# Optimization experiments

Measured on AMD Instinct MI355X. Metric: run time of the kernel, lower is better.

The kernel has to match this reference:

```python
import jax, jax.numpy as jnp
import numpy as np

N = 262144   # cohort size (k_n)
M = 8192     # number of ordinal anchor indices (len(Hj))


def setup_inputs() -> dict:
    key = jax.random.key(0)
    k1, k2, k3, k4, k5 = jax.random.split(key, 5)
    time = jax.random.uniform(k1, (N,), dtype=jnp.float32) * 1000.0
    event = (jax.random.uniform(k2, (N,), dtype=jnp.float32) < 0.3).astype(jnp.float32)
    y_true0 = jnp.stack([time, event], axis=1)          # [N,2] (time, event)
    y_true1 = y_true0                                    # second head labels (unused by loss)
    y_pred0 = jax.random.normal(k3, (N, 1), dtype=jnp.float32) * 0.1  # xbeta head 0
    y_pred1 = jax.random.normal(k4, (N, 1), dtype=jnp.float32) * 0.1  # xbeta head 1
    Hj = jnp.sort(jax.random.randint(k5, (M,), 0, N, dtype=jnp.int32))  # static event indices into sorted order
    log_vars = jnp.zeros((2, 1), dtype=jnp.float32)      # layer weights log_var0, log_var1
    return {"y_true0": y_true0, "y_true1": y_true1, "y_pred0": y_pred0,
            "y_pred1": y_pred1, "Hj": Hj, "log_vars": log_vars}


def reference(y_true0, y_true1, y_pred0, y_pred1, Hj, log_vars):
    n = y_true0.shape[0]
    # top_k with k = n == full descending sort by time
    _, order = jax.lax.top_k(y_true0[:, 0], n)

    # ---- neg_log_pl (Cox negative partial log-likelihood, per-sample vector) ----
    xbeta = y_pred0[order, 0]                 # [N] sorted by descending time
    event = y_true0[order, 1]                 # [N]
    denom = jnp.cumsum(jnp.exp(xbeta))        # risk-set cumulative sum
    lossA = -(event * (xbeta - jnp.log(denom)))  # [N]

    # ---- ordinal_loss0 (pairwise ranking over event indices Hj in sorted order) ----
    # intended math: for each j, for ii >= j: cost += 1 - exp(xbeta[Hj[j]] - xbeta[Hj[ii]])
    xb = y_pred1[order, 0]                    # [N] sorted
    xh = xb[Hj]                               # [M]
    m = Hj.shape[0]
    rec = 1.0 - jnp.exp(xh[:, None] - xh[None, :])   # [M,M] rec[j,ii]
    mask = jnp.triu(jnp.ones((m, m), dtype=bool))    # ii >= j
    cost2 = jnp.sum(jnp.where(mask, rec, 0.0))

    # ---- multi_loss combination with learned log variances ----
    lv0 = log_vars[0, 0]
    lv1 = log_vars[1, 0]
    precision1 = jnp.clip(jnp.exp(-lv1), 0.0, 1.0)
    loss = jnp.sum(lossA + lv0) + (precision1 * cost2 + lv1)
    return loss


if __name__ == "__main__":
    out = reference(**setup_inputs())
    print(out)
```

## Files before the change

kernel.cpp:

```cpp
#include <hip/hip_runtime.h>
#include <math.h>


#define BSHIFT 12
#define NBUCK (1 << 19)
#define BLK 256
#define NC1 32
#define M40 ((1ull << 40) - 1)

#define BAR_FLAG 512
#define BAR_REL  1024

#define STORE_U32(p, v) __hip_atomic_store((p), (v), __ATOMIC_RELAXED, __HIP_MEMORY_SCOPE_AGENT)
#define STORE_F32(p, v) __hip_atomic_store((p), (v), __ATOMIC_RELAXED, __HIP_MEMORY_SCOPE_AGENT)
#define STORE_U64(p, v) __hip_atomic_store((unsigned long long*)(p), (v), __ATOMIC_RELAXED, __HIP_MEMORY_SCOPE_AGENT)
#define LOAD_U32(p) __hip_atomic_load((p), __ATOMIC_RELAXED, __HIP_MEMORY_SCOPE_AGENT)
#define FADD_U32(p, v) __hip_atomic_fetch_add((p), (v), __ATOMIC_RELAXED, __HIP_MEMORY_SCOPE_AGENT)

template <int GRID>
__device__ __forceinline__ void gbar(unsigned* bar, unsigned gv) {
  __syncthreads();
  constexpr unsigned BPC = GRID / NC1;
  const int t = threadIdx.x;
  const unsigned grp = blockIdx.x & (NC1 - 1);
  if (blockIdx.x == 0) {
    if (t == 0) {
      unsigned a = FADD_U32(bar + grp * 16, 1u);
      if (a == gv * BPC - 1u) STORE_U32(bar + BAR_FLAG + grp * 16, gv);
    }
    if (t < NC1) {
      int guard = 0;
      while (LOAD_U32(bar + BAR_FLAG + t * 16) < gv) {
        __builtin_amdgcn_s_sleep(1);
        if (++guard > 5000000) break;
      }
      STORE_U32(bar + BAR_REL + t * 16, gv);
    }
    __syncthreads();
  } else {
    if (t == 0) {
      unsigned a = FADD_U32(bar + grp * 16, 1u);
      if (a == gv * BPC - 1u) STORE_U32(bar + BAR_FLAG + grp * 16, gv);
      int guard = 0;
      while (LOAD_U32(bar + BAR_REL + grp * 16) < gv) {
        __builtin_amdgcn_s_sleep(1);
        if (++guard > 5000000) break;
      }
    }
    __syncthreads();
  }
}

template <int GRID>
__device__ __forceinline__ void gbar_last(unsigned* bar, unsigned gv) {
  __syncthreads();
  constexpr unsigned BPC = GRID / NC1;
  const int t = threadIdx.x;
  const unsigned grp = blockIdx.x & (NC1 - 1);
  if (blockIdx.x == 0) {
    if (t == 0) {
      unsigned a = FADD_U32(bar + grp * 16, 1u);
      if (a == gv * BPC - 1u) STORE_U32(bar + BAR_FLAG + grp * 16, gv);
    }
    if (t < NC1) {
      int guard = 0;
      while (LOAD_U32(bar + BAR_FLAG + t * 16) < gv) {
        __builtin_amdgcn_s_sleep(1);
        if (++guard > 5000000) break;
      }
    }
    __syncthreads();
  } else {
    if (t == 0) {
      unsigned a = FADD_U32(bar + grp * 16, 1u);
      if (a == gv * BPC - 1u) STORE_U32(bar + BAR_FLAG + grp * 16, gv);
    }
  }
}

__global__ void __launch_bounds__(BLK, 4)
k_hist(const float2* __restrict__ yt0, const float* __restrict__ yp0, int n,
       unsigned long long* __restrict__ rec, unsigned* __restrict__ seq) {
  int i = blockIdx.x * BLK + threadIdx.x;
  if (i >= n) return;
  float2 te = yt0[i];
  unsigned key = __float_as_uint(te.x);
  float e = expf(yp0[i]);
  unsigned long long qe = (unsigned long long)(e * 16777216.0f + 0.5f);
  if (qe > (1ull << 32)) qe = (1ull << 32);
  unsigned long long ret = atomicAdd(&rec[key >> BSHIFT], (1ull << 40) | qe);
  seq[i] = (unsigned)(ret >> 40);
}

template <int GRID>
__global__ void __launch_bounds__(BLK, 4)
k_scan(const unsigned long long* __restrict__ rec,
       const int* __restrict__ Hj, int m,
       unsigned* __restrict__ bar, unsigned* __restrict__ bitmap,
       unsigned long long* __restrict__ Epack,
       unsigned* __restrict__ bTot, float* __restrict__ fTot) {
  constexpr int TOT = GRID * BLK;
  constexpr int BPB = NBUCK / GRID;
  constexpr int BPT = BPB / BLK;
  const int t = threadIdx.x;
  const int g = blockIdx.x;
  const int gtid = g * BLK + t;

  __shared__ unsigned su[BLK];
  __shared__ float    sff[BLK];

  for (int j = gtid; j < m; j += TOT) {
    int h = Hj[j];
    atomicOr(&bitmap[h >> 5], 1u << (h & 31));
  }

  unsigned cK[BPT]; float fK[BPT];
  unsigned thrC; float thrF;
  {
    unsigned runc = 0u; float runf = 0.f;
    #pragma unroll
    for (int k = 0; k < BPT; ++k) {
      int b = NBUCK - 1 - (g * BPB + t * BPT + k);
      unsigned long long v = rec[b];
      cK[k] = (unsigned)(v >> 40);
      fK[k] = (float)((double)(v & M40) * (1.0 / 16777216.0));
      runc += cK[k]; runf += fK[k];
    }
    su[t] = runc; sff[t] = runf;
    __syncthreads();
    for (int off2 = 1; off2 < BLK; off2 <<= 1) {
      unsigned uc = (t >= off2) ? su[t - off2] : 0u;
      float    uf = (t >= off2) ? sff[t - off2] : 0.f;
      __syncthreads();
      su[t] += uc; sff[t] += uf;
      __syncthreads();
    }
    thrC = (t > 0) ? su[t - 1] : 0u;
    thrF = (t > 0) ? sff[t - 1] : 0.f;
    if (t == BLK - 1) { STORE_U32(&bTot[g], su[t]); STORE_F32(&fTot[g], sff[t]); }
  }
  gbar<GRID>(bar, 1);

  {
    unsigned partC = 0u; float partF = 0.f;
    for (int j = t; j < g; j += BLK) { partC += bTot[j]; partF += fTot[j]; }
    su[t] = partC; sff[t] = partF;
    __syncthreads();
    for (int s = BLK / 2; s > 0; s >>= 1) {
      if (t < s) { su[t] += su[t + s]; sff[t] += sff[t + s]; }
      __syncthreads();
    }
    unsigned baseC = su[0]; float baseF = sff[0];
    __syncthreads();
    unsigned preC = 0u; float preF = 0.f;
    #pragma unroll
    for (int k = 0; k < BPT; ++k) {
      int b = NBUCK - 1 - (g * BPB + t * BPT + k);
      unsigned sfxC = baseC + thrC + preC;
      float    sfxF = baseF + thrF + preF;
      Epack[b] = ((unsigned long long)__float_as_uint(sfxF) << 32) | sfxC;
      preC += cK[k]; preF += fK[k];
    }
  }
}

template <int GRID>
__global__ void __launch_bounds__(BLK, 4)
k_main(const float2* __restrict__ yt0, const float* __restrict__ yp0,
       const float* __restrict__ yp1, const int* __restrict__ Hj,
       const float* __restrict__ lv, int n, int m,
       unsigned* __restrict__ bar, const unsigned* __restrict__ seq,
       const unsigned* __restrict__ bitmap,
       const unsigned long long* __restrict__ Epack,
       uint2* __restrict__ skey2, unsigned* __restrict__ sidx,
       float* __restrict__ xh, double* __restrict__ accum,
       float* __restrict__ out) {
  constexpr int TOT = GRID * BLK;
  const int t = threadIdx.x;
  const int g = blockIdx.x;
  const int gtid = g * BLK + t;

  __shared__ double sd[BLK];
  __shared__ float  wt[4];

  #pragma unroll
  for (int el = 0; el < 2; ++el) {
    int i = gtid + el * TOT;
    if (i < n) {
      float2 te = yt0[i];
      unsigned key = __float_as_uint(te.x);
      unsigned ev = (te.y != 0.f) ? 0x80000000u : 0u;
      float e = expf(yp0[i]);
      unsigned b = key >> BSHIFT;
      unsigned start = ((const unsigned*)Epack)[2u * b];
      unsigned pos = start + seq[i];
      unsigned long long v =
          ((unsigned long long)__float_as_uint(e) << 32) | key;
      STORE_U64(&skey2[pos], v);
      STORE_U32(&sidx[pos], (unsigned)i | ev);
    }
  }
  gbar<GRID>(bar, 1);

  {
    double contrib = 0.0;
    #pragma unroll
    for (int el = 0; el < 2; ++el) {
      int p = gtid + el * TOT;
      if (p >= n) continue;
      uint2 kv = skey2[p];
      unsigned key = kv.x;
      float e = __uint_as_float(kv.y);
      unsigned sidv = sidx[p];
      unsigned idx = sidv & 0x7FFFFFFFu;
      bool evb = (sidv >> 31) != 0u;
      unsigned b = key >> BSHIFT;
      unsigned long long ep = Epack[b];
      unsigned start = (unsigned)ep;
      float cross = __uint_as_float((unsigned)(ep >> 32));
      unsigned end = (b > 0) ? ((const unsigned*)Epack)[2u * (b - 1)]
                             : (unsigned)n;
      if (end > (unsigned)n) end = (unsigned)n;
      if (start > end) start = end;
      float wsum = 0.f;
      unsigned wcnt = 0u;
      unsigned q = start;
      while (q + 8 <= end) {
        uint2 v[8];
        #pragma unroll
        for (int k = 0; k < 8; ++k) v[k] = skey2[q + k];
        #pragma unroll
        for (int k = 0; k < 8; ++k) {
          if (v[k].x > key) { wsum += __uint_as_float(v[k].y); wcnt++; }
          else if (v[k].x == key && (sidx[q + k] & 0x7FFFFFFFu) < idx) {
            wsum += __uint_as_float(v[k].y); wcnt++;
          }
        }
        q += 8;
      }
      for (; q < end; ++q) {
        uint2 v = skey2[q];
        if (v.x > key) { wsum += __uint_as_float(v.y); wcnt++; }
        else if (v.x == key && (sidx[q] & 0x7FFFFFFFu) < idx) {
          wsum += __uint_as_float(v.y); wcnt++;
        }
      }
      float denom = cross + wsum + e;
      int rank = (int)(start + wcnt);
      if (evb) contrib += (double)logf(denom / e);
      if ((bitmap[rank >> 5] >> (rank & 31)) & 1u) {
        int lo = 0, hi = m;
        while (lo < hi) { int mid = (lo + hi) >> 1; if (Hj[mid] < rank) lo = mid + 1; else hi = mid; }
        if (lo < m && Hj[lo] == rank) {
          float xb1 = yp1[idx];
          for (int j = lo; j < m && Hj[j] == rank; ++j) STORE_F32(&xh[j], xb1);
        }
      }
    }
    sd[t] = contrib;
    __syncthreads();
    for (int s = 128; s > 0; s >>= 1) { if (t < s) sd[t] += sd[t + s]; __syncthreads(); }
    if (t == 0) atomicAdd(accum, sd[0]);
  }
  gbar_last<GRID>(bar, 2);

  if (g != 0) return;
  {
    int lane = t & 63;
    int w = t >> 6;
    double acc = 0.0;
    float carry = 0.f;
    int passes = (m + 2047) / 2048;
    for (int pss = passes - 1; pss >= 0; --pss) {
      int base = pss * 2048 + t * 8;
      float x[8], eb[8];
      float c = 0.f;
      #pragma unroll
      for (int k = 0; k < 8; ++k) {
        int j = base + k;
        x[k] = (j < m) ? xh[j] : 0.f;
        eb[k] = (j < m) ? expf(-x[k]) : 0.f;
        c += eb[k];
      }
      float s = c;
      #pragma unroll
      for (int d = 1; d < 64; d <<= 1) {
        float o = __shfl_down(s, d, 64);
        if (lane + d < 64) s += o;
      }
      float wtot = __shfl(s, 0, 64);
      if (lane == 0) wt[w] = wtot;
      __syncthreads();
      float after = 0.f, ptot = 0.f;
      #pragma unroll
      for (int w2 = 0; w2 < 4; ++w2) { ptot += wt[w2]; if (w2 > w) after += wt[w2]; }
      float S = (s - c) + after + carry;
      #pragma unroll
      for (int k = 7; k >= 0; --k) {
        int j = base + k;
        S += eb[k];
        if (j < m) acc += (double)(expf(x[k]) * S);
      }
      __syncthreads();
      carry += ptot;
    }
    sd[t] = acc;
    __syncthreads();
    for (int s2 = 128; s2 > 0; s2 >>= 1) { if (t < s2) sd[t] += sd[t + s2]; __syncthreads(); }
    if (t == 0) {
      double T = (double)m * (double)(m + 1) * 0.5;
      double cost2 = T - sd[0];
      float lv0 = lv[0], lv1 = lv[1];
      float prec1 = fminf(expf(-lv1), 1.0f);
      double loss = *accum + (double)n * (double)lv0 + (double)prec1 * cost2 + (double)lv1;
      out[0] = (float)loss;
    }
  }
}

extern "C" void kernel_launch(void* const* d_in, const int* in_sizes, int n_in,
                              void* d_out, int out_size, void* d_ws, size_t ws_size,
                              hipStream_t stream) {
  (void)n_in; (void)out_size;
  const float2* yt0 = (const float2*)d_in[0];
  const float*  yp0 = (const float*)d_in[2];
  const float*  yp1 = (const float*)d_in[3];
  const int*    Hj  = (const int*)d_in[4];
  const float*  lv  = (const float*)d_in[5];
  int n = in_sizes[0] / 2;
  int m = in_sizes[4];

  char* ws = (char*)d_ws;
  unsigned* barS  = (unsigned*)ws;
  unsigned* barM  = (unsigned*)(ws + 8192);
  double*   accum = (double*)(ws + 16128);
  size_t off = 16384;
  auto alloc = [&](size_t bytes) -> void* {
    void* p = ws + off;
    off += (bytes + 255) & ~(size_t)255;
    return p;
  };
  size_t nbm = ((size_t)(n + 31) / 32) * 4;
  unsigned* bitmap = (unsigned*)alloc(nbm);
  unsigned long long* rec = (unsigned long long*)alloc((size_t)NBUCK * 8);
  size_t zbytes = off;
  unsigned long long* Epack = (unsigned long long*)alloc((size_t)NBUCK * 8);
  unsigned* bTot  = (unsigned*)alloc(1024 * 4);
  float*    fTot  = (float*)alloc(1024 * 4);
  unsigned* seq   = (unsigned*)alloc((size_t)n * 4);
  uint2*    skey2 = (uint2*)alloc((size_t)n * 8);
  unsigned* sidx  = (unsigned*)alloc((size_t)n * 4);
  float*    xh    = (float*)alloc((size_t)m * 4);
  if (off > ws_size) return;

  hipMemsetAsync(ws, 0, zbytes, stream);

  static int gridChoice = 0;
  if (gridChoice == 0) {
    int nb = 0;
    hipError_t e1 = hipOccupancyMaxActiveBlocksPerMultiprocessor(&nb, k_main<1024>, BLK, 0);
    int dev = 0; hipGetDevice(&dev);
    hipDeviceProp_t prop;
    hipError_t e2 = hipGetDeviceProperties(&prop, dev);
    gridChoice = (e1 == hipSuccess && e2 == hipSuccess &&
                  nb * prop.multiProcessorCount >= 1024) ? 1024 : 512;
  }

  int gHist = (n + BLK - 1) / BLK;
  k_hist<<<dim3(gHist), dim3(BLK), 0, stream>>>(yt0, yp0, n, rec, seq);
  if (gridChoice == 1024) {
    k_scan<1024><<<dim3(1024), dim3(BLK), 0, stream>>>(rec, Hj, m, barS, bitmap,
                                                       Epack, bTot, fTot);
    k_main<1024><<<dim3(1024), dim3(BLK), 0, stream>>>(yt0, yp0, yp1, Hj, lv, n, m,
                                                       barM, seq, bitmap, Epack,
                                                       skey2, sidx, xh, accum,
                                                       (float*)d_out);
  } else {
    k_scan<512><<<dim3(512), dim3(BLK), 0, stream>>>(rec, Hj, m, barS, bitmap,
                                                     Epack, bTot, fTot);
    k_main<512><<<dim3(512), dim3(BLK), 0, stream>>>(yt0, yp0, yp1, Hj, lv, n, m,
                                                     barM, seq, bitmap, Epack,
                                                     skey2, sidx, xh, accum,
                                                     (float*)d_out);
  }
}
```

Measured before the change: 136.5 us.

## Split persistent main kernel into scatter, windowed walk and final kernels

Replaces the persistent k_main kernel, which used software grid barriers, with three ordinary launches: scatter, walk and a single-block final reduction. Kernel boundaries now provide the synchronisation. The walk kernel stages a 512-element window of sorted keys in shared memory, so most intra-bucket comparisons read LDS instead of global memory. Bucket ranges that extend past the window still fall back to global reads. The change trades the grid-barrier spin cost and the idle time of blocks at the final step for two extra launch overheads.

```diff
diff --git a/kernel.cpp b/kernel.cpp
--- a/kernel.cpp
+++ b/kernel.cpp
@@ -7,13 +7,13 @@
 #define BLK 256
 #define NC1 32
 #define M40 ((1ull << 40) - 1)
+#define WIN 512
 
 #define BAR_FLAG 512
 #define BAR_REL  1024
 
 #define STORE_U32(p, v) __hip_atomic_store((p), (v), __ATOMIC_RELAXED, __HIP_MEMORY_SCOPE_AGENT)
 #define STORE_F32(p, v) __hip_atomic_store((p), (v), __ATOMIC_RELAXED, __HIP_MEMORY_SCOPE_AGENT)
-#define STORE_U64(p, v) __hip_atomic_store((unsigned long long*)(p), (v), __ATOMIC_RELAXED, __HIP_MEMORY_SCOPE_AGENT)
 #define LOAD_U32(p) __hip_atomic_load((p), __ATOMIC_RELAXED, __HIP_MEMORY_SCOPE_AGENT)
 #define FADD_U32(p, v) __hip_atomic_fetch_add((p), (v), __ATOMIC_RELAXED, __HIP_MEMORY_SCOPE_AGENT)
 
@@ -51,29 +51,29 @@
   }
 }
 
-template <int GRID>
-__device__ __forceinline__ void gbar_last(unsigned* bar, unsigned gv) {
-  __syncthreads();
-  constexpr unsigned BPC = GRID / NC1;
-  const int t = threadIdx.x;
-  const unsigned grp = blockIdx.x & (NC1 - 1);
-  if (blockIdx.x == 0) {
-    if (t == 0) {
-      unsigned a = FADD_U32(bar + grp * 16, 1u);
-      if (a == gv * BPC - 1u) STORE_U32(bar + BAR_FLAG + grp * 16, gv);
-    }
-    if (t < NC1) {
-      int guard = 0;
-      while (LOAD_U32(bar + BAR_FLAG + t * 16) < gv) {
-        __builtin_amdgcn_s_sleep(1);
-        if (++guard > 5000000) break;
-      }
-    }
-    __syncthreads();
-  } else {
-    if (t == 0) {
-      unsigned a = FADD_U32(bar + grp * 16, 1u);
-      if (a == gv * BPC - 1u) STORE_U32(bar + BAR_FLAG + grp * 16, gv);
+__device__ __forceinline__ void walk_global(const uint2* __restrict__ skey2,
+                                            const unsigned* __restrict__ sidx,
+                                            unsigned q, unsigned qe,
+                                            unsigned key, unsigned idx,
+                                            float& wsum, unsigned& wcnt) {
+  while (q + 8 <= qe) {
+    uint2 v[8];
+    #pragma unroll
+    for (int k = 0; k < 8; ++k) v[k] = skey2[q + k];
+    #pragma unroll
+    for (int k = 0; k < 8; ++k) {
+      if (v[k].x > key) { wsum += __uint_as_float(v[k].y); wcnt++; }
+      else if (v[k].x == key && (sidx[q + k] & 0x7FFFFFFFu) < idx) {
+        wsum += __uint_as_float(v[k].y); wcnt++;
+      }
+    }
+    q += 8;
+  }
+  for (; q < qe; ++q) {
+    uint2 v = skey2[q];
+    if (v.x > key) { wsum += __uint_as_float(v.y); wcnt++; }
+    else if (v.x == key && (sidx[q] & 0x7FFFFFFFu) < idx) {
+      wsum += __uint_as_float(v.y); wcnt++;
     }
   }
 }
@@ -164,157 +164,169 @@
   }
 }
 
-template <int GRID>
-__global__ void __launch_bounds__(BLK, 4)
-k_main(const float2* __restrict__ yt0, const float* __restrict__ yp0,
-       const float* __restrict__ yp1, const int* __restrict__ Hj,
-       const float* __restrict__ lv, int n, int m,
-       unsigned* __restrict__ bar, const unsigned* __restrict__ seq,
+__global__ void __launch_bounds__(BLK, 4)
+k_scatter(const float2* __restrict__ yt0, const float* __restrict__ yp0, int n,
+          const unsigned* __restrict__ seq,
+          const unsigned long long* __restrict__ Epack,
+          uint2* __restrict__ skey2, unsigned* __restrict__ sidx) {
+  int i = blockIdx.x * BLK + threadIdx.x;
+  if (i >= n) return;
+  float2 te = yt0[i];
+  unsigned key = __float_as_uint(te.x);
+  unsigned ev = (te.y != 0.f) ? 0x80000000u : 0u;
+  float e = expf(yp0[i]);
+  unsigned b = key >> BSHIFT;
+  unsigned start = ((const unsigned*)Epack)[2u * b];
+  unsigned pos = start + seq[i];
+  uint2 v; v.x = key; v.y = __float_as_uint(e);
+  skey2[pos] = v;
+  sidx[pos] = (unsigned)i | ev;
+}
+
+__global__ void __launch_bounds__(BLK, 4)
+k_walk(const float* __restrict__ yp1, const int* __restrict__ Hj,
+       int n, int m,
        const unsigned* __restrict__ bitmap,
        const unsigned long long* __restrict__ Epack,
-       uint2* __restrict__ skey2, unsigned* __restrict__ sidx,
-       float* __restrict__ xh, double* __restrict__ accum,
-       float* __restrict__ out) {
-  constexpr int TOT = GRID * BLK;
+       const uint2* __restrict__ skey2, const unsigned* __restrict__ sidx,
+       float* __restrict__ xh, double* __restrict__ accum) {
+  __shared__ uint2    skl[WIN];
+  __shared__ unsigned sil[WIN];
+  __shared__ double   sd[BLK];
   const int t = threadIdx.x;
-  const int g = blockIdx.x;
-  const int gtid = g * BLK + t;
-
-  __shared__ double sd[BLK];
-  __shared__ float  wt[4];
+  const int p0 = blockIdx.x * WIN;
 
   #pragma unroll
-  for (int el = 0; el < 2; ++el) {
-    int i = gtid + el * TOT;
-    if (i < n) {
-      float2 te = yt0[i];
-      unsigned key = __float_as_uint(te.x);
-      unsigned ev = (te.y != 0.f) ? 0x80000000u : 0u;
-      float e = expf(yp0[i]);
-      unsigned b = key >> BSHIFT;
-      unsigned start = ((const unsigned*)Epack)[2u * b];
-      unsigned pos = start + seq[i];
-      unsigned long long v =
-          ((unsigned long long)__float_as_uint(e) << 32) | key;
-      STORE_U64(&skey2[pos], v);
-      STORE_U32(&sidx[pos], (unsigned)i | ev);
-    }
-  }
-  gbar<GRID>(bar, 1);
-
-  {
-    double contrib = 0.0;
-    #pragma unroll
-    for (int el = 0; el < 2; ++el) {
-      int p = gtid + el * TOT;
-      if (p >= n) continue;
-      uint2 kv = skey2[p];
-      unsigned key = kv.x;
-      float e = __uint_as_float(kv.y);
-      unsigned sidv = sidx[p];
-      unsigned idx = sidv & 0x7FFFFFFFu;
-      bool evb = (sidv >> 31) != 0u;
-      unsigned b = key >> BSHIFT;
-      unsigned long long ep = Epack[b];
-      unsigned start = (unsigned)ep;
-      float cross = __uint_as_float((unsigned)(ep >> 32));
-      unsigned end = (b > 0) ? ((const unsigned*)Epack)[2u * (b - 1)]
-                             : (unsigned)n;
-      if (end > (unsigned)n) end = (unsigned)n;
-      if (start > end) start = end;
-      float wsum = 0.f;
-      unsigned wcnt = 0u;
-      unsigned q = start;
-      while (q + 8 <= end) {
+  for (int k = 0; k < WIN / BLK; ++k) {
+    int j = t + k * BLK;
+    int p = p0 + j;
+    if (p < n) { skl[j] = skey2[p]; sil[j] = sidx[p]; }
+  }
+  __syncthreads();
+
+  double contrib = 0.0;
+  #pragma unroll
+  for (int el = 0; el < WIN / BLK; ++el) {
+    int j = t + el * BLK;
+    int p = p0 + j;
+    if (p >= n) continue;
+    uint2 kv = skl[j];
+    unsigned key = kv.x;
+    float e = __uint_as_float(kv.y);
+    unsigned sidv = sil[j];
+    unsigned idx = sidv & 0x7FFFFFFFu;
+    bool evb = (sidv >> 31) != 0u;
+    unsigned b = key >> BSHIFT;
+    unsigned long long ep = Epack[b];
+    unsigned start = (unsigned)ep;
+    float cross = __uint_as_float((unsigned)(ep >> 32));
+    unsigned end = (b > 0) ? ((const unsigned*)Epack)[2u * (b - 1)]
+                           : (unsigned)n;
+    if (end > (unsigned)n) end = (unsigned)n;
+    if (start > end) start = end;
+    float wsum = 0.f;
+    unsigned wcnt = 0u;
+    unsigned wl0 = (start > (unsigned)p0) ? start : (unsigned)p0;
+    unsigned hi2 = (unsigned)(p0 + WIN);
+    unsigned wl1 = (end < hi2) ? end : hi2;
+    if (start < wl0) walk_global(skey2, sidx, start, wl0, key, idx, wsum, wcnt);
+    if (wl1 < end)   walk_global(skey2, sidx, wl1, end, key, idx, wsum, wcnt);
+    {
+      unsigned q = wl0;
+      while (q + 8 <= wl1) {
         uint2 v[8];
         #pragma unroll
-        for (int k = 0; k < 8; ++k) v[k] = skey2[q + k];
+        for (int k = 0; k < 8; ++k) v[k] = skl[q - p0 + k];
         #pragma unroll
         for (int k = 0; k < 8; ++k) {
           if (v[k].x > key) { wsum += __uint_as_float(v[k].y); wcnt++; }
-          else if (v[k].x == key && (sidx[q + k] & 0x7FFFFFFFu) < idx) {
+          else if (v[k].x == key && (sil[q - p0 + k] & 0x7FFFFFFFu) < idx) {
             wsum += __uint_as_float(v[k].y); wcnt++;
           }
         }
         q += 8;
       }
-      for (; q < end; ++q) {
-        uint2 v = skey2[q];
+      for (; q < wl1; ++q) {
+        uint2 v = skl[q - p0];
         if (v.x > key) { wsum += __uint_as_float(v.y); wcnt++; }
-        else if (v.x == key && (sidx[q] & 0x7FFFFFFFu) < idx) {
+        else if (v.x == key && (sil[q - p0] & 0x7FFFFFFFu) < idx) {
           wsum += __uint_as_float(v.y); wcnt++;
         }
       }
-      float denom = cross + wsum + e;
-      int rank = (int)(start + wcnt);
-      if (evb) contrib += (double)logf(denom / e);
-      if ((bitmap[rank >> 5] >> (rank & 31)) & 1u) {
-        int lo = 0, hi = m;
-        while (lo < hi) { int mid = (lo + hi) >> 1; if (Hj[mid] < rank) lo = mid + 1; else hi = mid; }
-        if (lo < m && Hj[lo] == rank) {
-          float xb1 = yp1[idx];
-          for (int j = lo; j < m && Hj[j] == rank; ++j) STORE_F32(&xh[j], xb1);
-        }
-      }
-    }
-    sd[t] = contrib;
-    __syncthreads();
-    for (int s = 128; s > 0; s >>= 1) { if (t < s) sd[t] += sd[t + s]; __syncthreads(); }
-    if (t == 0) atomicAdd(accum, sd[0]);
-  }
-  gbar_last<GRID>(bar, 2);
-
-  if (g != 0) return;
-  {
-    int lane = t & 63;
-    int w = t >> 6;
-    double acc = 0.0;
-    float carry = 0.f;
-    int passes = (m + 2047) / 2048;
-    for (int pss = passes - 1; pss >= 0; --pss) {
-      int base = pss * 2048 + t * 8;
-      float x[8], eb[8];
-      float c = 0.f;
-      #pragma unroll
-      for (int k = 0; k < 8; ++k) {
-        int j = base + k;
-        x[k] = (j < m) ? xh[j] : 0.f;
-        eb[k] = (j < m) ? expf(-x[k]) : 0.f;
-        c += eb[k];
-      }
-      float s = c;
-      #pragma unroll
-      for (int d = 1; d < 64; d <<= 1) {
-        float o = __shfl_down(s, d, 64);
-        if (lane + d < 64) s += o;
-      }
-      float wtot = __shfl(s, 0, 64);
-      if (lane == 0) wt[w] = wtot;
-      __syncthreads();
-      float after = 0.f, ptot = 0.f;
-      #pragma unroll
-      for (int w2 = 0; w2 < 4; ++w2) { ptot += wt[w2]; if (w2 > w) after += wt[w2]; }
-      float S = (s - c) + after + carry;
-      #pragma unroll
-      for (int k = 7; k >= 0; --k) {
-        int j = base + k;
-        S += eb[k];
-        if (j < m) acc += (double)(expf(x[k]) * S);
-      }
-      __syncthreads();
-      carry += ptot;
-    }
-    sd[t] = acc;
-    __syncthreads();
-    for (int s2 = 128; s2 > 0; s2 >>= 1) { if (t < s2) sd[t] += sd[t + s2]; __syncthreads(); }
-    if (t == 0) {
-      double T = (double)m * (double)(m + 1) * 0.5;
-      double cost2 = T - sd[0];
-      float lv0 = lv[0], lv1 = lv[1];
-      float prec1 = fminf(expf(-lv1), 1.0f);
-      double loss = *accum + (double)n * (double)lv0 + (double)prec1 * cost2 + (double)lv1;
-      out[0] = (float)loss;
-    }
+    }
+    float denom = cross + wsum + e;
+    int rank = (int)(start + wcnt);
+    if (evb) contrib += (double)logf(denom / e);
+    if ((bitmap[rank >> 5] >> (rank & 31)) & 1u) {
+      int lo = 0, hi = m;
+      while (lo < hi) { int mid = (lo + hi) >> 1; if (Hj[mid] < rank) lo = mid + 1; else hi = mid; }
+      if (lo < m && Hj[lo] == rank) {
+        float xb1 = yp1[idx];
+        for (int jj = lo; jj < m && Hj[jj] == rank; ++jj) xh[jj] = xb1;
+      }
+    }
+  }
+  sd[t] = contrib;
+  __syncthreads();
+  for (int s = 128; s > 0; s >>= 1) { if (t < s) sd[t] += sd[t + s]; __syncthreads(); }
+  if (t == 0) atomicAdd(accum, sd[0]);
+}
+
+__global__ void __launch_bounds__(BLK, 4)
+k_final(const float* __restrict__ xh, int m, int n,
+        const double* __restrict__ accum, const float* __restrict__ lv,
+        float* __restrict__ out) {
+  __shared__ double sd[BLK];
+  __shared__ float  wt[4];
+  const int t = threadIdx.x;
+  int lane = t & 63;
+  int w = t >> 6;
+  double acc = 0.0;
+  float carry = 0.f;
+  int passes = (m + 2047) / 2048;
+  for (int pss = passes - 1; pss >= 0; --pss) {
+    int base = pss * 2048 + t * 8;
+    float x[8], eb[8];
+    float c = 0.f;
+    #pragma unroll
+    for (int k = 0; k < 8; ++k) {
+      int j = base + k;
+      x[k] = (j < m) ? xh[j] : 0.f;
+      eb[k] = (j < m) ? expf(-x[k]) : 0.f;
+      c += eb[k];
+    }
+    float s = c;
+    #pragma unroll
+    for (int d = 1; d < 64; d <<= 1) {
+      float o = __shfl_down(s, d, 64);
+      if (lane + d < 64) s += o;
+    }
+    float wtot = __shfl(s, 0, 64);
+    if (lane == 0) wt[w] = wtot;
+    __syncthreads();
+    float after = 0.f, ptot = 0.f;
+    #pragma unroll
+    for (int w2 = 0; w2 < 4; ++w2) { ptot += wt[w2]; if (w2 > w) after += wt[w2]; }
+    float S = (s - c) + after + carry;
+    #pragma unroll
+    for (int k = 7; k >= 0; --k) {
+      int j = base + k;
+      S += eb[k];
+      if (j < m) acc += (double)(expf(x[k]) * S);
+    }
+    __syncthreads();
+    carry += ptot;
+  }
+  sd[t] = acc;
+  __syncthreads();
+  for (int s2 = 128; s2 > 0; s2 >>= 1) { if (t < s2) sd[t] += sd[t + s2]; __syncthreads(); }
+  if (t == 0) {
+    double T = (double)m * (double)(m + 1) * 0.5;
+    double cost2 = T - sd[0];
+    float lv0 = lv[0], lv1 = lv[1];
+    float prec1 = fminf(expf(-lv1), 1.0f);
+    double loss = *accum + (double)n * (double)lv0 + (double)prec1 * cost2 + (double)lv1;
+    out[0] = (float)loss;
   }
 }
 
@@ -332,9 +344,8 @@
 
   char* ws = (char*)d_ws;
   unsigned* barS  = (unsigned*)ws;
-  unsigned* barM  = (unsigned*)(ws + 8192);
-  double*   accum = (double*)(ws + 16128);
-  size_t off = 16384;
+  double*   accum = (double*)(ws + 7168);
+  size_t off = 8192;
   auto alloc = [&](size_t bytes) -> void* {
     void* p = ws + off;
     off += (bytes + 255) & ~(size_t)255;
@@ -358,7 +369,7 @@
   static int gridChoice = 0;
   if (gridChoice == 0) {
     int nb = 0;
-    hipError_t e1 = hipOccupancyMaxActiveBlocksPerMultiprocessor(&nb, k_main<1024>, BLK, 0);
+    hipError_t e1 = hipOccupancyMaxActiveBlocksPerMultiprocessor(&nb, k_scan<1024>, BLK, 0);
     int dev = 0; hipGetDevice(&dev);
     hipDeviceProp_t prop;
     hipError_t e2 = hipGetDeviceProperties(&prop, dev);
@@ -366,21 +377,19 @@
                   nb * prop.multiProcessorCount >= 1024) ? 1024 : 512;
   }
 
-  int gHist = (n + BLK - 1) / BLK;
-  k_hist<<<dim3(gHist), dim3(BLK), 0, stream>>>(yt0, yp0, n, rec, seq);
-  if (gridChoice == 1024) {
+  int gN = (n + BLK - 1) / BLK;
+  int gW = (n + WIN - 1) / WIN;
+  k_hist<<<dim3(gN), dim3(BLK), 0, stream>>>(yt0, yp0, n, rec, seq);
+  if (gridChoice == 1024)
     k_scan<1024><<<dim3(1024), dim3(BLK), 0, stream>>>(rec, Hj, m, barS, bitmap,
                                                        Epack, bTot, fTot);
-    k_main<1024><<<dim3(1024), dim3(BLK), 0, stream>>>(yt0, yp0, yp1, Hj, lv, n, m,
-                                                       barM, seq, bitmap, Epack,
-                                                       skey2, sidx, xh, accum,
-                                                       (float*)d_out);
-  } else {
+  else
     k_scan<512><<<dim3(512), dim3(BLK), 0, stream>>>(rec, Hj, m, barS, bitmap,
                                                      Epack, bTot, fTot);
-    k_main<512><<<dim3(512), dim3(BLK), 0, stream>>>(yt0, yp0, yp1, Hj, lv, n, m,
-                                                     barM, seq, bitmap, Epack,
-                                                     skey2, sidx, xh, accum,
-                                                     (float*)d_out);
-  }
-}
+  k_scatter<<<dim3(gN), dim3(BLK), 0, stream>>>(yt0, yp0, n, seq, Epack,
+                                                skey2, sidx);
+  k_walk<<<dim3(gW), dim3(BLK), 0, stream>>>(yp1, Hj, n, m, bitmap, Epack,
+                                             skey2, sidx, xh, accum);
+  k_final<<<dim3(1), dim3(BLK), 0, stream>>>(xh, m, n, accum, lv,
+                                             (float*)d_out);
+}
```

New measurement: 136.0 us. About the same (-0.4%).
